# Performance work log

Measured on AMD Instinct MI355X. Metric: run time of the kernel, lower is better.

## Reference

```python
import jax, jax.numpy as jnp
import numpy as np

H = 64          # HIDDEN_DIM
V = 64          # VOCAB_SIZE
LN_EPS = 1e-5   # torch LayerNorm default
D_EPS = 1e-6    # denom epsilon in delta rule
MEM_SCALE = 1.0 # forward default arg


def setup_inputs() -> dict:
    key = jax.random.key(0)
    ks = jax.random.split(key, 8)
    B, L = 16, 2048
    s = lambda k, shape: (jax.random.normal(k, shape, jnp.float32) * 0.05)
    return {
        "seq": jax.random.randint(ks[0], (B, L), 0, V),
        "embed": s(ks[1], (V, H)),
        "W1": s(ks[2], (H, 2 * H)), "b1": jnp.zeros((2 * H,), jnp.float32),
        "W2": s(ks[3], (2 * H, H)), "b2": jnp.zeros((H,), jnp.float32),
        "gamma": jnp.ones((H,), jnp.float32), "beta": jnp.zeros((H,), jnp.float32),
        "Wr": s(ks[4], (H, H)), "br": jnp.zeros((H,), jnp.float32),
        "Wo": s(ks[5], (H, V)), "bo": jnp.zeros((V,), jnp.float32),
    }


def reference(seq, embed, W1, b1, W2, b2, gamma, beta, Wr, br, Wo, bo):
    h = embed[seq]                                  # (B, L, H)
    ff = jax.nn.relu(h @ W1 + b1) @ W2 + b2         # (B, L, H)
    x = h + ff
    mu = x.mean(-1, keepdims=True)
    var = x.var(-1, keepdims=True)                  # biased, as torch LayerNorm
    h = (x - mu) / jnp.sqrt(var + LN_EPS) * gamma + beta

    B = h.shape[0]
    keys = jnp.swapaxes(h[:, :-1, :], 0, 1)         # (L-1, B, H): all but last token

    def step(M, k):                                  # M: (B, H, H), k: (B, H)
        v_pred = jnp.einsum('bij,bj->bi', M, k)
        denom = (k * k).sum(-1, keepdims=True) + D_EPS
        dv = k - v_pred / denom
        M = M + MEM_SCALE * dv[:, :, None] * k[:, None, :]
        return M, None

    M0 = jnp.zeros((B, H, H), h.dtype)
    M, _ = jax.lax.scan(step, M0, keys)

    q = h[:, -1, :]                                  # last token as query
    ctx = jnp.einsum('bij,bj->bi', M, q)             # (B, H)
    return (ctx @ Wr + br) @ Wo + bo                 # (B, V)
```

## Files before the change

### kernel.cpp

```cpp
#include <hip/hip_runtime.h>

#define HDIM 64
#define LSEQ 2048
#define BATCH 16
#define LN_EPS 1e-5f
#define D_EPS 1e-6f
#define NSEG 32
#define CPS 4

typedef unsigned short u16;
typedef unsigned int   u32;

__device__ __forceinline__ float bf2f(u16 v) {
    return __uint_as_float(((u32)v) << 16);
}
__device__ __forceinline__ u16 f2bf(float f) {
    u32 u = __float_as_uint(f);
    return (u16)((u + 0x7FFFu + ((u >> 16) & 1u)) >> 16);
}

#define A_SW1   0
#define A_SW2   16896
#define A_ET    34304
#define A_HIDT  51712
#define A_RED1  69120
#define A_RED2  70176
#define A_SMU   71232
#define A_SRSTD 71504
#define H_ROWS  71776
#define H_INVD  80480
#define SMEM_BYTES 80736
#define C_S     0
#define C_V     17408
#define C_BM    34816
#define C_Z     39168
#define C_GM    43520

__global__ __launch_bounds__(256, 2) void fused_pc_kernel(
    const int* __restrict__ seq, const float* __restrict__ embed,
    const float* __restrict__ W1, const float* __restrict__ b1,
    const float* __restrict__ W2, const float* __restrict__ b2,
    const float* __restrict__ gamma, const float* __restrict__ beta,
    u32* __restrict__ PK, u16* __restrict__ q_ws)
{
    __shared__ __align__(16) char smem[SMEM_BYTES];
    const int t = threadIdx.x;
    const int b = blockIdx.x >> 5;
    const int s = blockIdx.x & 31;
    const int tok0 = 1984 - 64 * s;

    u16*   hrows  = (u16*)(smem + H_ROWS);
    float* invd_l = (float*)(smem + H_INVD);

    {
        u16*   sW1   = (u16*)(smem + A_SW1);
        u16*   sW2   = (u16*)(smem + A_SW2);
        float* eT    = (float*)(smem + A_ET);
        u16*   hidT  = (u16*)(smem + A_HIDT);
        float* red1  = (float*)(smem + A_RED1);
        float* red2  = (float*)(smem + A_RED2);
        float* smu   = (float*)(smem + A_SMU);
        float* srstd = (float*)(smem + A_SRSTD);

        {
            const float4* s1 = (const float4*)W1;
#pragma unroll
            for (int q = 0; q < 8; ++q) {
                const int m = t + 256 * q;
                const int row = m >> 5, col = m & 31;
                const float4 v = s1[m];
                ushort4 w;
                w.x = f2bf(v.x); w.y = f2bf(v.y); w.z = f2bf(v.z); w.w = f2bf(v.w);
                *(ushort4*)&sW1[row * 132 + col * 4] = w;
            }
            const float4* s2 = (const float4*)W2;
#pragma unroll
            for (int q = 0; q < 8; ++q) {
                const int m = t + 256 * q;
                const int row = m >> 4, col = m & 15;
                const float4 v = s2[m];
                ushort4 w;
                w.x = f2bf(v.x); w.y = f2bf(v.y); w.z = f2bf(v.z); w.w = f2bf(v.w);
                *(ushort4*)&sW2[row * 68 + col * 4] = w;
            }
        }
        {
            const int tk = t >> 2, p = t & 3;
            const int v = seq[b * LSEQ + tok0 + tk];
            const float* er = embed + v * HDIM + 16 * p;
#pragma unroll
            for (int q = 0; q < 4; ++q) {
                const float4 ev = *(const float4*)(er + 4 * q);
                const int d = 16 * p + 4 * q;
                eT[(d + 0) * 68 + tk] = ev.x;
                eT[(d + 1) * 68 + tk] = ev.y;
                eT[(d + 2) * 68 + tk] = ev.z;
                eT[(d + 3) * 68 + tk] = ev.w;
            }
        }
        __syncthreads();

        const int r = t >> 4;
        const int c = t & 15;

        {
            float acc0[4][4], acc1[4][4];
#pragma unroll
            for (int o = 0; o < 4; ++o) {
                const float bA = b1[4 * c + o];
                const float bB = b1[64 + 4 * c + o];
#pragma unroll
                for (int j = 0; j < 4; ++j) { acc0[j][o] = bA; acc1[j][o] = bB; }
            }
            for (int k = 0; k < 64; ++k) {
                const float4  ev = *(const float4*)&eT[k * 68 + 4 * r];
                const ushort4 wa = *(const ushort4*)&sW1[k * 132 + 4 * c];
                const ushort4 wb = *(const ushort4*)&sW1[k * 132 + 64 + 4 * c];
                const float e4[4] = {ev.x, ev.y, ev.z, ev.w};
                const float a4[4] = {bf2f(wa.x), bf2f(wa.y), bf2f(wa.z), bf2f(wa.w)};
                const float b4[4] = {bf2f(wb.x), bf2f(wb.y), bf2f(wb.z), bf2f(wb.w)};
#pragma unroll
                for (int j = 0; j < 4; ++j)
#pragma unroll
                    for (int o = 0; o < 4; ++o) {
                        acc0[j][o] = fmaf(e4[j], a4[o], acc0[j][o]);
                        acc1[j][o] = fmaf(e4[j], b4[o], acc1[j][o]);
                    }
            }
#pragma unroll
            for (int o = 0; o < 4; ++o) {
                ushort4 v0, v1;
                v0.x = f2bf(fmaxf(acc0[0][o], 0.f)); v0.y = f2bf(fmaxf(acc0[1][o], 0.f));
                v0.z = f2bf(fmaxf(acc0[2][o], 0.f)); v0.w = f2bf(fmaxf(acc0[3][o], 0.f));
                *(ushort4*)&hidT[(4 * c + o) * 68 + 4 * r] = v0;
                v1.x = f2bf(fmaxf(acc1[0][o], 0.f)); v1.y = f2bf(fmaxf(acc1[1][o], 0.f));
                v1.z = f2bf(fmaxf(acc1[2][o], 0.f)); v1.w = f2bf(fmaxf(acc1[3][o], 0.f));
                *(ushort4*)&hidT[(64 + 4 * c + o) * 68 + 4 * r] = v1;
            }
        }
        __syncthreads();

        {
            float acc[4][4];
#pragma unroll
            for (int o = 0; o < 4; ++o) {
                const float bv = b2[4 * c + o];
#pragma unroll
                for (int j = 0; j < 4; ++j) acc[j][o] = bv;
            }
            for (int k = 0; k < 128; ++k) {
                const ushort4 hv = *(const ushort4*)&hidT[k * 68 + 4 * r];
                const ushort4 wv = *(const ushort4*)&sW2[k * 68 + 4 * c];
                const float h4[4] = {bf2f(hv.x), bf2f(hv.y), bf2f(hv.z), bf2f(hv.w)};
                const float w4[4] = {bf2f(wv.x), bf2f(wv.y), bf2f(wv.z), bf2f(wv.w)};
#pragma unroll
                for (int j = 0; j < 4; ++j)
#pragma unroll
                    for (int o = 0; o < 4; ++o)
                        acc[j][o] = fmaf(h4[j], w4[o], acc[j][o]);
            }
#pragma unroll
            for (int o = 0; o < 4; ++o) {
                float4 ex = *(float4*)&eT[(4 * c + o) * 68 + 4 * r];
                ex.x += acc[0][o];
                ex.y += acc[1][o];
                ex.z += acc[2][o];
                ex.w += acc[3][o];
                *(float4*)&eT[(4 * c + o) * 68 + 4 * r] = ex;
            }
        }
        __syncthreads();

        {
            const int tk = t & 63, p = t >> 6;
            float sv = 0.f, q = 0.f;
#pragma unroll
            for (int i = 0; i < 16; ++i) {
                const float x = eT[(16 * p + i) * 68 + tk];
                sv += x;
                q = fmaf(x, x, q);
            }
            red1[p * 66 + tk] = sv;
            red2[p * 66 + tk] = q;
        }
        __syncthreads();
        if (t < 64) {
            const float sv = ((red1[0 * 66 + t] + red1[1 * 66 + t]) + (red1[2 * 66 + t] + red1[3 * 66 + t]));
            const float qq = ((red2[0 * 66 + t] + red2[1 * 66 + t]) + (red2[2 * 66 + t] + red2[3 * 66 + t]));
            const float mu  = sv * (1.0f / 64.0f);
            const float var = qq * (1.0f / 64.0f) - mu * mu;
            smu[t]   = mu;
            srstd[t] = 1.0f / sqrtf(var + LN_EPS);
        }
        __syncthreads();

        {
            const int tk = t >> 2, p = t & 3;
            const float mu = smu[tk], rstd = srstd[tk];
            float hh = 0.f;
#pragma unroll
            for (int i2 = 0; i2 < 8; ++i2) {
                const int d = 16 * p + 2 * i2;
                const float x0 = eT[(d + 0) * 68 + tk];
                const float x1 = eT[(d + 1) * 68 + tk];
                const float o0 = (x0 - mu) * rstd * gamma[d + 0] + beta[d + 0];
                const float o1 = (x1 - mu) * rstd * gamma[d + 1] + beta[d + 1];
                const u16 r0 = f2bf(o0), r1 = f2bf(o1);
                const float q0f = bf2f(r0), q1f = bf2f(r1);
                hh = fmaf(q0f, q0f, hh);
                hh = fmaf(q1f, q1f, hh);
                *(u32*)&hrows[tk * 68 + d] = (u32)r0 | ((u32)r1 << 16);
                if (s == 0 && tk == 63) {
                    q_ws[b * 64 + d]     = r0;
                    q_ws[b * 64 + d + 1] = r1;
                }
            }
            red1[p * 66 + tk] = hh;
        }
        __syncthreads();
        if (t < 64) {
            const float hh = ((red1[0 * 66 + t] + red1[1 * 66 + t]) + (red1[2 * 66 + t] + red1[3 * 66 + t]));
            invd_l[t] = 1.0f / (hh + D_EPS);
        }
    }
    __syncthreads();

    if (s == 0 && t < 64) hrows[63 * 68 + t] = 0;

    {
        float* S  = (float*)(smem + C_S);
        float* V  = (float*)(smem + C_V);
        float* Bm = (float*)(smem + C_BM);
        float* Z  = (float*)(smem + C_Z);
        float* Gm = (float*)(smem + C_GM);

        for (int idx = t; idx < 64 * 64; idx += 256) {
            const int m = idx >> 6, n = idx & 63;
            S[m * 68 + n] = (m == n) ? 1.0f : 0.0f;
            V[m * 68 + n] = 0.0f;
        }

        for (int cc = 0; cc < CPS; ++cc) {
            const int base = 63 - 16 * cc;
            __syncthreads();

            {
                const int i = t >> 4, j = t & 15;
                if (i > j) {
                    const u16* ra = &hrows[(base - i) * 68];
                    const u16* rb = &hrows[(base - j) * 68];
                    float acc = 0.f;
#pragma unroll
                    for (int m = 0; m < 64; m += 4) {
                        const ushort4 a4 = *(const ushort4*)&ra[m];
                        const ushort4 b4 = *(const ushort4*)&rb[m];
                        acc += bf2f(a4.x) * bf2f(b4.x) + bf2f(a4.y) * bf2f(b4.y)
                             + bf2f(a4.z) * bf2f(b4.z) + bf2f(a4.w) * bf2f(b4.w);
                    }
                    Gm[i * 17 + j] = acc * invd_l[base - j];
                }
            }
            __syncthreads();

            if (t < 64) {
                const int n = t;
                float Breg[16];
#pragma unroll
                for (int i = 0; i < 16; ++i) {
                    float acc = bf2f(hrows[(base - i) * 68 + n]);
#pragma unroll
                    for (int j = 0; j < 16; ++j)
                        if (j < i) acc = fmaf(-Gm[i * 17 + j], Breg[j], acc);
                    Breg[i] = acc;
                    Bm[i * 68 + n] = acc;
                }
            }
            __syncthreads();

            {
                const int i  = t & 15;
                const int n0 = (t >> 4) * 4;
                float4 z = make_float4(0.f, 0.f, 0.f, 0.f);
#pragma unroll
                for (int mq = 0; mq < 16; ++mq) {
                    const float4 bq = *(const float4*)&Bm[i * 68 + mq * 4];
                    const float4 s0 = *(const float4*)&S[(mq * 4 + 0) * 68 + n0];
                    const float4 s1 = *(const float4*)&S[(mq * 4 + 1) * 68 + n0];
                    const float4 s2 = *(const float4*)&S[(mq * 4 + 2) * 68 + n0];
                    const float4 s3 = *(const float4*)&S[(mq * 4 + 3) * 68 + n0];
                    z.x = fmaf(bq.x, s0.x, fmaf(bq.y, s1.x, fmaf(bq.z, s2.x, fmaf(bq.w, s3.x, z.x))));
                    z.y = fmaf(bq.x, s0.y, fmaf(bq.y, s1.y, fmaf(bq.z, s2.y, fmaf(bq.w, s3.y, z.y))));
                    z.z = fmaf(bq.x, s0.z, fmaf(bq.y, s1.z, fmaf(bq.z, s2.z, fmaf(bq.w, s3.z, z.z))));
                    z.w = fmaf(bq.x, s0.w, fmaf(bq.y, s1.w, fmaf(bq.z, s2.w, fmaf(bq.w, s3.w, z.w))));
                }
                *(float4*)&Z[i * 68 + n0] = z;
            }
            __syncthreads();

            {
                const int n0 = (t & 15) * 4;
                const int mh = t >> 4;
                float iv16[16];
#pragma unroll
                for (int q4 = 0; q4 < 4; ++q4) {
                    const float4 v4 = *(const float4*)&invd_l[base - 15 + 4 * q4];
                    iv16[15 - 4 * q4]     = v4.x;
                    iv16[15 - 4 * q4 - 1] = v4.y;
                    iv16[15 - 4 * q4 - 2] = v4.z;
                    iv16[15 - 4 * q4 - 3] = v4.w;
                }
                float4 sacc[4], vacc[4];
#pragma unroll
                for (int p = 0; p < 4; ++p) {
                    sacc[p] = *(float4*)&S[(mh + 16 * p) * 68 + n0];
                    vacc[p] = *(float4*)&V[(mh + 16 * p) * 68 + n0];
                }
#pragma unroll
                for (int j = 0; j < 16; ++j) {
                    const float4 zq = *(const float4*)&Z[j * 68 + n0];
                    const float iv = iv16[j];
                    float4 ztq;
                    ztq.x = zq.x * iv; ztq.y = zq.y * iv;
                    ztq.z = zq.z * iv; ztq.w = zq.w * iv;
                    const u16* kr = &hrows[(base - j) * 68];
                    const float k0 = bf2f(kr[mh]);
                    const float k1 = bf2f(kr[mh + 16]);
                    const float k2 = bf2f(kr[mh + 32]);
                    const float k3 = bf2f(kr[mh + 48]);
                    vacc[0].x = fmaf(k0, zq.x, vacc[0].x); vacc[0].y = fmaf(k0, zq.y, vacc[0].y);
                    vacc[0].z = fmaf(k0, zq.z, vacc[0].z); vacc[0].w = fmaf(k0, zq.w, vacc[0].w);
                    vacc[1].x = fmaf(k1, zq.x, vacc[1].x); vacc[1].y = fmaf(k1, zq.y, vacc[1].y);
                    vacc[1].z = fmaf(k1, zq.z, vacc[1].z); vacc[1].w = fmaf(k1, zq.w, vacc[1].w);
                    vacc[2].x = fmaf(k2, zq.x, vacc[2].x); vacc[2].y = fmaf(k2, zq.y, vacc[2].y);
                    vacc[2].z = fmaf(k2, zq.z, vacc[2].z); vacc[2].w = fmaf(k2, zq.w, vacc[2].w);
                    vacc[3].x = fmaf(k3, zq.x, vacc[3].x); vacc[3].y = fmaf(k3, zq.y, vacc[3].y);
                    vacc[3].z = fmaf(k3, zq.z, vacc[3].z); vacc[3].w = fmaf(k3, zq.w, vacc[3].w);
                    sacc[0].x = fmaf(-k0, ztq.x, sacc[0].x); sacc[0].y = fmaf(-k0, ztq.y, sacc[0].y);
                    sacc[0].z = fmaf(-k0, ztq.z, sacc[0].z); sacc[0].w = fmaf(-k0, ztq.w, sacc[0].w);
                    sacc[1].x = fmaf(-k1, ztq.x, sacc[1].x); sacc[1].y = fmaf(-k1, ztq.y, sacc[1].y);
                    sacc[1].z = fmaf(-k1, ztq.z, sacc[1].z); sacc[1].w = fmaf(-k1, ztq.w, sacc[1].w);
                    sacc[2].x = fmaf(-k2, ztq.x, sacc[2].x); sacc[2].y = fmaf(-k2, ztq.y, sacc[2].y);
                    sacc[2].z = fmaf(-k2, ztq.z, sacc[2].z); sacc[2].w = fmaf(-k2, ztq.w, sacc[2].w);
                    sacc[3].x = fmaf(-k3, ztq.x, sacc[3].x); sacc[3].y = fmaf(-k3, ztq.y, sacc[3].y);
                    sacc[3].z = fmaf(-k3, ztq.z, sacc[3].z); sacc[3].w = fmaf(-k3, ztq.w, sacc[3].w);
                }
#pragma unroll
                for (int p = 0; p < 4; ++p) {
                    *(float4*)&S[(mh + 16 * p) * 68 + n0] = sacc[p];
                    *(float4*)&V[(mh + 16 * p) * 68 + n0] = vacc[p];
                }
            }
        }
        __syncthreads();

        u32* pk = PK + ((size_t)(b * NSEG + s) << 12);
        for (int idx = t; idx < 4096; idx += 256) {
            const int j = idx >> 6, i = idx & 63;
            const u32 sb = ((u32)f2bf(S[i * 68 + j])) << 16;
            const u32 vb = (u32)f2bf(V[i * 68 + j]);
            pk[idx] = sb | vb;
        }
    }
}

__global__ __launch_bounds__(256, 1) void final_kernel(
    const u16* __restrict__ q_ws, const u32* __restrict__ PK,
    const float* __restrict__ Wr, const float* __restrict__ br,
    const float* __restrict__ Wo, const float* __restrict__ bo,
    float* __restrict__ out)
{
    const int b    = blockIdx.x;
    const int t    = threadIdx.x;
    const int lane = t & 63;
    const int p    = t >> 6;

    __shared__ float psum[4][72];
    __shared__ float rl[64];
    __shared__ float cs[64], rs[64];

    rl[lane] = bf2f(q_ws[b * 64 + lane]);

    float ctxp = 0.f;
    u32 cur[16], nxt[16];
    {
        const u32* pk0 = PK + ((size_t)(b * NSEG + 0) << 12);
#pragma unroll
        for (int jj = 0; jj < 16; ++jj)
            cur[jj] = pk0[(p * 16 + jj) * 64 + lane];
    }
    __syncthreads();

    for (int s = 0; s < NSEG; ++s) {
        const int sn = (s + 1 < NSEG) ? s + 1 : s;
        const u32* pkn = PK + ((size_t)(b * NSEG + sn) << 12);
#pragma unroll
        for (int jj = 0; jj < 16; ++jj)
            nxt[jj] = pkn[(p * 16 + jj) * 64 + lane];

        float accr = 0.f;
#pragma unroll
        for (int jj = 0; jj < 16; ++jj) {
            const u32 pv = cur[jj];
            const float Sv = __uint_as_float(pv & 0xFFFF0000u);
            const float Vv = __uint_as_float(pv << 16);
            const float rj = rl[p * 16 + jj];
            accr = fmaf(Sv, rj, accr);
            ctxp = fmaf(Vv, rj, ctxp);
        }
        psum[p][lane] = accr;
        __syncthreads();
        const float rn = (psum[0][lane] + psum[1][lane]) + (psum[2][lane] + psum[3][lane]);
        __syncthreads();
        rl[lane] = rn;

#pragma unroll
        for (int jj = 0; jj < 16; ++jj) cur[jj] = nxt[jj];
    }

    psum[p][lane] = ctxp;
    __syncthreads();
    if (t < 64)
        cs[t] = (psum[0][t] + psum[1][t]) + (psum[2][t] + psum[3][t]);
    __syncthreads();

    float rv = (p == 0) ? br[lane] : 0.f;
#pragma unroll
    for (int i = 0; i < 16; ++i)
        rv = fmaf(cs[p * 16 + i], Wr[(p * 16 + i) * HDIM + lane], rv);
    psum[p][lane] = rv;
    __syncthreads();
    if (t < 64)
        rs[t] = (psum[0][t] + psum[1][t]) + (psum[2][t] + psum[3][t]);
    __syncthreads();

    float ov = (p == 0) ? bo[lane] : 0.f;
#pragma unroll
    for (int i = 0; i < 16; ++i)
        ov = fmaf(rs[p * 16 + i], Wo[(p * 16 + i) * HDIM + lane], ov);
    psum[p][lane] = ov;
    __syncthreads();
    if (t < 64)
        out[(size_t)b * HDIM + t] = (psum[0][t] + psum[1][t]) + (psum[2][t] + psum[3][t]);
}

extern "C" void kernel_launch(void* const* d_in, const int* in_sizes, int n_in,
                              void* d_out, int out_size, void* d_ws, size_t ws_size,
                              hipStream_t stream)
{
    const int*   seq   = (const int*)  d_in[0];
    const float* embed = (const float*)d_in[1];
    const float* W1    = (const float*)d_in[2];
    const float* b1    = (const float*)d_in[3];
    const float* W2    = (const float*)d_in[4];
    const float* b2    = (const float*)d_in[5];
    const float* gamma = (const float*)d_in[6];
    const float* beta  = (const float*)d_in[7];
    const float* Wr    = (const float*)d_in[8];
    const float* br    = (const float*)d_in[9];
    const float* Wo    = (const float*)d_in[10];
    const float* bo    = (const float*)d_in[11];

    u32* pk_ws = (u32*)d_ws;
    u16* q_ws  = (u16*)(pk_ws + (size_t)BATCH * NSEG * 4096);
    float* outp = (float*)d_out;

    hipLaunchKernelGGL(fused_pc_kernel, dim3(BATCH * NSEG), dim3(256), 0, stream,
                       seq, embed, W1, b1, W2, b2, gamma, beta, pk_ws, q_ws);
    hipLaunchKernelGGL(final_kernel, dim3(BATCH), dim3(256), 0, stream,
                       q_ws, pk_ws, Wr, br, Wo, bo, outp);
}
```

Baseline: 138.6 us.

## Compute prologue FFN with bf16 MFMA and warp-shuffle LayerNorm reductions

The two feed-forward matmuls in the per-block prologue move from scalar FMA tiles to __builtin_amdgcn_mfma_f32_16x16x32_bf16. To support this, the weights and hidden activations are stored in shared memory in an MFMA fragment layout, and each wave handles 16 tokens. LayerNorm statistics and the delta-rule denominators are now reduced with cross-lane shuffles inside a wave instead of shared-memory reduction arrays, which removes several __syncthreads and shrinks LDS use. The embedding input is now rounded to bf16 before the first matmul, which may change numerics slightly.

```diff
diff --git a/kernel.cpp b/kernel.cpp
--- a/kernel.cpp
+++ b/kernel.cpp
@@ -10,6 +10,8 @@
 
 typedef unsigned short u16;
 typedef unsigned int   u32;
+typedef __attribute__((ext_vector_type(8))) short bf16x8;
+typedef __attribute__((ext_vector_type(4))) float f32x4;
 
 __device__ __forceinline__ float bf2f(u16 v) {
     return __uint_as_float(((u32)v) << 16);
@@ -19,17 +21,13 @@
     return (u16)((u + 0x7FFFu + ((u >> 16) & 1u)) >> 16);
 }
 
-#define A_SW1   0
-#define A_SW2   16896
-#define A_ET    34304
-#define A_HIDT  51712
-#define A_RED1  69120
-#define A_RED2  70176
-#define A_SMU   71232
-#define A_SRSTD 71504
-#define H_ROWS  71776
-#define H_INVD  80480
-#define SMEM_BYTES 80736
+#define A_W1F  0
+#define A_W2F  16384
+#define A_ER   32768
+#define A_HF   50176
+#define H_ROWS 66560
+#define H_INVD 75264
+#define SMEM_BYTES 75520
 #define C_S     0
 #define C_V     17408
 #define C_BM    34816
@@ -53,35 +51,41 @@
     float* invd_l = (float*)(smem + H_INVD);
 
     {
-        u16*   sW1   = (u16*)(smem + A_SW1);
-        u16*   sW2   = (u16*)(smem + A_SW2);
-        float* eT    = (float*)(smem + A_ET);
-        u16*   hidT  = (u16*)(smem + A_HIDT);
-        float* red1  = (float*)(smem + A_RED1);
-        float* red2  = (float*)(smem + A_RED2);
-        float* smu   = (float*)(smem + A_SMU);
-        float* srstd = (float*)(smem + A_SRSTD);
+        u16*   sW1f = (u16*)(smem + A_W1F);
+        u16*   sW2f = (u16*)(smem + A_W2F);
+        float* eR   = (float*)(smem + A_ER);
+        u16*   hF   = (u16*)(smem + A_HF);
 
         {
             const float4* s1 = (const float4*)W1;
 #pragma unroll
             for (int q = 0; q < 8; ++q) {
                 const int m = t + 256 * q;
-                const int row = m >> 5, col = m & 31;
+                const int k = m >> 5;
+                const int o0 = (m & 31) * 4;
                 const float4 v = s1[m];
-                ushort4 w;
-                w.x = f2bf(v.x); w.y = f2bf(v.y); w.z = f2bf(v.z); w.w = f2bf(v.w);
-                *(ushort4*)&sW1[row * 132 + col * 4] = w;
+                const float e4[4] = {v.x, v.y, v.z, v.w};
+                const int ks = k >> 5, l4 = ((k >> 3) & 3) << 4, i = k & 7;
+#pragma unroll
+                for (int e = 0; e < 4; ++e) {
+                    const int o = o0 + e;
+                    sW1f[((ks * 8 + (o >> 4)) * 64 + l4 + (o & 15)) * 8 + i] = f2bf(e4[e]);
+                }
             }
             const float4* s2 = (const float4*)W2;
 #pragma unroll
             for (int q = 0; q < 8; ++q) {
                 const int m = t + 256 * q;
-                const int row = m >> 4, col = m & 15;
+                const int k = m >> 4;
+                const int o0 = (m & 15) * 4;
                 const float4 v = s2[m];
-                ushort4 w;
-                w.x = f2bf(v.x); w.y = f2bf(v.y); w.z = f2bf(v.z); w.w = f2bf(v.w);
-                *(ushort4*)&sW2[row * 68 + col * 4] = w;
+                const float e4[4] = {v.x, v.y, v.z, v.w};
+                const int ks = k >> 5, l4 = ((k >> 3) & 3) << 4, i = k & 7;
+#pragma unroll
+                for (int e = 0; e < 4; ++e) {
+                    const int o = o0 + e;
+                    sW2f[((ks * 4 + (o >> 4)) * 64 + l4 + (o & 15)) * 8 + i] = f2bf(e4[e]);
+                }
             }
         }
         {
@@ -89,138 +93,117 @@
             const int v = seq[b * LSEQ + tok0 + tk];
             const float* er = embed + v * HDIM + 16 * p;
 #pragma unroll
-            for (int q = 0; q < 4; ++q) {
-                const float4 ev = *(const float4*)(er + 4 * q);
-                const int d = 16 * p + 4 * q;
-                eT[(d + 0) * 68 + tk] = ev.x;
-                eT[(d + 1) * 68 + tk] = ev.y;
-                eT[(d + 2) * 68 + tk] = ev.z;
-                eT[(d + 3) * 68 + tk] = ev.w;
-            }
+            for (int q = 0; q < 4; ++q)
+                *(float4*)&eR[tk * 68 + 16 * p + 4 * q] = *(const float4*)(er + 4 * q);
         }
         __syncthreads();
 
-        const int r = t >> 4;
-        const int c = t & 15;
-
-        {
-            float acc0[4][4], acc1[4][4];
-#pragma unroll
-            for (int o = 0; o < 4; ++o) {
-                const float bA = b1[4 * c + o];
-                const float bB = b1[64 + 4 * c + o];
-#pragma unroll
-                for (int j = 0; j < 4; ++j) { acc0[j][o] = bA; acc1[j][o] = bB; }
-            }
-            for (int k = 0; k < 64; ++k) {
-                const float4  ev = *(const float4*)&eT[k * 68 + 4 * r];
-                const ushort4 wa = *(const ushort4*)&sW1[k * 132 + 4 * c];
-                const ushort4 wb = *(const ushort4*)&sW1[k * 132 + 64 + 4 * c];
-                const float e4[4] = {ev.x, ev.y, ev.z, ev.w};
-                const float a4[4] = {bf2f(wa.x), bf2f(wa.y), bf2f(wa.z), bf2f(wa.w)};
-                const float b4[4] = {bf2f(wb.x), bf2f(wb.y), bf2f(wb.z), bf2f(wb.w)};
-#pragma unroll
-                for (int j = 0; j < 4; ++j)
-#pragma unroll
-                    for (int o = 0; o < 4; ++o) {
-                        acc0[j][o] = fmaf(e4[j], a4[o], acc0[j][o]);
-                        acc1[j][o] = fmaf(e4[j], b4[o], acc1[j][o]);
-                    }
-            }
-#pragma unroll
-            for (int o = 0; o < 4; ++o) {
-                ushort4 v0, v1;
-                v0.x = f2bf(fmaxf(acc0[0][o], 0.f)); v0.y = f2bf(fmaxf(acc0[1][o], 0.f));
-                v0.z = f2bf(fmaxf(acc0[2][o], 0.f)); v0.w = f2bf(fmaxf(acc0[3][o], 0.f));
-                *(ushort4*)&hidT[(4 * c + o) * 68 + 4 * r] = v0;
-                v1.x = f2bf(fmaxf(acc1[0][o], 0.f)); v1.y = f2bf(fmaxf(acc1[1][o], 0.f));
-                v1.z = f2bf(fmaxf(acc1[2][o], 0.f)); v1.w = f2bf(fmaxf(acc1[3][o], 0.f));
-                *(ushort4*)&hidT[(64 + 4 * c + o) * 68 + 4 * r] = v1;
-            }
-        }
-        __syncthreads();
-
-        {
-            float acc[4][4];
-#pragma unroll
-            for (int o = 0; o < 4; ++o) {
-                const float bv = b2[4 * c + o];
-#pragma unroll
-                for (int j = 0; j < 4; ++j) acc[j][o] = bv;
-            }
-            for (int k = 0; k < 128; ++k) {
-                const ushort4 hv = *(const ushort4*)&hidT[k * 68 + 4 * r];
-                const ushort4 wv = *(const ushort4*)&sW2[k * 68 + 4 * c];
-                const float h4[4] = {bf2f(hv.x), bf2f(hv.y), bf2f(hv.z), bf2f(hv.w)};
-                const float w4[4] = {bf2f(wv.x), bf2f(wv.y), bf2f(wv.z), bf2f(wv.w)};
-#pragma unroll
-                for (int j = 0; j < 4; ++j)
-#pragma unroll
-                    for (int o = 0; o < 4; ++o)
-                        acc[j][o] = fmaf(h4[j], w4[o], acc[j][o]);
-            }
-#pragma unroll
-            for (int o = 0; o < 4; ++o) {
-                float4 ex = *(float4*)&eT[(4 * c + o) * 68 + 4 * r];
-                ex.x += acc[0][o];
-                ex.y += acc[1][o];
-                ex.z += acc[2][o];
-                ex.w += acc[3][o];
-                *(float4*)&eT[(4 * c + o) * 68 + 4 * r] = ex;
-            }
-        }
-        __syncthreads();
-
-        {
-            const int tk = t & 63, p = t >> 6;
-            float sv = 0.f, q = 0.f;
-#pragma unroll
-            for (int i = 0; i < 16; ++i) {
-                const float x = eT[(16 * p + i) * 68 + tk];
-                sv += x;
-                q = fmaf(x, x, q);
-            }
-            red1[p * 66 + tk] = sv;
-            red2[p * 66 + tk] = q;
-        }
-        __syncthreads();
-        if (t < 64) {
-            const float sv = ((red1[0 * 66 + t] + red1[1 * 66 + t]) + (red1[2 * 66 + t] + red1[3 * 66 + t]));
-            const float qq = ((red2[0 * 66 + t] + red2[1 * 66 + t]) + (red2[2 * 66 + t] + red2[3 * 66 + t]));
-            const float mu  = sv * (1.0f / 64.0f);
-            const float var = qq * (1.0f / 64.0f) - mu * mu;
-            smu[t]   = mu;
-            srstd[t] = 1.0f / sqrtf(var + LN_EPS);
-        }
-        __syncthreads();
-
-        {
-            const int tk = t >> 2, p = t & 3;
-            const float mu = smu[tk], rstd = srstd[tk];
-            float hh = 0.f;
-#pragma unroll
-            for (int i2 = 0; i2 < 8; ++i2) {
-                const int d = 16 * p + 2 * i2;
-                const float x0 = eT[(d + 0) * 68 + tk];
-                const float x1 = eT[(d + 1) * 68 + tk];
-                const float o0 = (x0 - mu) * rstd * gamma[d + 0] + beta[d + 0];
-                const float o1 = (x1 - mu) * rstd * gamma[d + 1] + beta[d + 1];
-                const u16 r0 = f2bf(o0), r1 = f2bf(o1);
-                const float q0f = bf2f(r0), q1f = bf2f(r1);
-                hh = fmaf(q0f, q0f, hh);
-                hh = fmaf(q1f, q1f, hh);
-                *(u32*)&hrows[tk * 68 + d] = (u32)r0 | ((u32)r1 << 16);
-                if (s == 0 && tk == 63) {
-                    q_ws[b * 64 + d]     = r0;
-                    q_ws[b * 64 + d + 1] = r1;
-                }
-            }
-            red1[p * 66 + tk] = hh;
-        }
-        __syncthreads();
-        if (t < 64) {
-            const float hh = ((red1[0 * 66 + t] + red1[1 * 66 + t]) + (red1[2 * 66 + t] + red1[3 * 66 + t]));
-            invd_l[t] = 1.0f / (hh + D_EPS);
+        const int lane = t & 63;
+        const int w    = t >> 6;
+        const int g    = lane >> 4;
+        const int c    = lane & 15;
+
+        bf16x8 ea[2];
+#pragma unroll
+        for (int ks = 0; ks < 2; ++ks) {
+            const float* src = &eR[(16 * w + c) * 68 + ks * 32 + g * 8];
+            const float4 v0 = *(const float4*)src;
+            const float4 v1 = *(const float4*)(src + 4);
+            bf16x8 f;
+            f[0] = (short)f2bf(v0.x); f[1] = (short)f2bf(v0.y);
+            f[2] = (short)f2bf(v0.z); f[3] = (short)f2bf(v0.w);
+            f[4] = (short)f2bf(v1.x); f[5] = (short)f2bf(v1.y);
+            f[6] = (short)f2bf(v1.z); f[7] = (short)f2bf(v1.w);
+            ea[ks] = f;
+        }
+
+#pragma unroll
+        for (int nt = 0; nt < 8; ++nt) {
+            const float bv = b1[16 * nt + c];
+            f32x4 acc = {bv, bv, bv, bv};
+#pragma unroll
+            for (int ks = 0; ks < 2; ++ks) {
+                const bf16x8 bf = *(const bf16x8*)&sW1f[((ks * 8 + nt) * 64 + lane) * 8];
+                acc = __builtin_amdgcn_mfma_f32_16x16x32_bf16(ea[ks], bf, acc, 0, 0, 0);
+            }
+            const int o   = 16 * nt + c;
+            const int ks2 = o >> 5;
+            const int l4  = ((o >> 3) & 3) << 4;
+            const int i   = o & 7;
+#pragma unroll
+            for (int r = 0; r < 4; ++r) {
+                const float hv = fmaxf(acc[r], 0.f);
+                hF[((w * 4 + ks2) * 64 + l4 + g * 4 + r) * 8 + i] = f2bf(hv);
+            }
+        }
+
+        bf16x8 ha[4];
+#pragma unroll
+        for (int ks = 0; ks < 4; ++ks)
+            ha[ks] = *(const bf16x8*)&hF[((w * 4 + ks) * 64 + lane) * 8];
+
+        float xf[4][4];
+#pragma unroll
+        for (int nt = 0; nt < 4; ++nt) {
+            const float bv = b2[16 * nt + c];
+            f32x4 acc = {bv, bv, bv, bv};
+#pragma unroll
+            for (int ks = 0; ks < 4; ++ks) {
+                const bf16x8 bf = *(const bf16x8*)&sW2f[((ks * 4 + nt) * 64 + lane) * 8];
+                acc = __builtin_amdgcn_mfma_f32_16x16x32_bf16(ha[ks], bf, acc, 0, 0, 0);
+            }
+#pragma unroll
+            for (int r = 0; r < 4; ++r)
+                xf[nt][r] = acc[r] + eR[(16 * w + g * 4 + r) * 68 + 16 * nt + c];
+        }
+
+        float s4[4] = {0, 0, 0, 0}, q4[4] = {0, 0, 0, 0};
+#pragma unroll
+        for (int nt = 0; nt < 4; ++nt)
+#pragma unroll
+            for (int r = 0; r < 4; ++r) {
+                s4[r] += xf[nt][r];
+                q4[r] = fmaf(xf[nt][r], xf[nt][r], q4[r]);
+            }
+#pragma unroll
+        for (int m = 1; m < 16; m <<= 1)
+#pragma unroll
+            for (int r = 0; r < 4; ++r) {
+                s4[r] += __shfl_xor(s4[r], m);
+                q4[r] += __shfl_xor(q4[r], m);
+            }
+        float mu[4], rstd[4];
+#pragma unroll
+        for (int r = 0; r < 4; ++r) {
+            mu[r] = s4[r] * (1.0f / 64.0f);
+            const float var = q4[r] * (1.0f / 64.0f) - mu[r] * mu[r];
+            rstd[r] = 1.0f / sqrtf(var + LN_EPS);
+        }
+
+        float hh[4] = {0, 0, 0, 0};
+#pragma unroll
+        for (int nt = 0; nt < 4; ++nt) {
+            const int o = 16 * nt + c;
+            const float gm = gamma[o], bt = beta[o];
+#pragma unroll
+            for (int r = 0; r < 4; ++r) {
+                const float ov = (xf[nt][r] - mu[r]) * rstd[r] * gm + bt;
+                const u16 rb = f2bf(ov);
+                const float qf = bf2f(rb);
+                hh[r] = fmaf(qf, qf, hh[r]);
+                hrows[(16 * w + g * 4 + r) * 68 + o] = rb;
+                if (s == 0 && w == 3 && g == 3 && r == 3)
+                    q_ws[b * 64 + o] = rb;
+            }
+        }
+#pragma unroll
+        for (int m = 1; m < 16; m <<= 1)
+#pragma unroll
+            for (int r = 0; r < 4; ++r) hh[r] += __shfl_xor(hh[r], m);
+        if (c == 0) {
+#pragma unroll
+            for (int r = 0; r < 4; ++r)
+                invd_l[16 * w + g * 4 + r] = 1.0f / (hh[r] + D_EPS);
         }
     }
     __syncthreads();
```

Measured after the change: 127.9 us. 7.7% less time.
